# Kernel tuning notes

Measured on AMD Instinct MI355X. Metric: run time of the kernel, lower is better.

Reference implementation:

```python
import jax, jax.numpy as jnp
import numpy as np

DIM = 1024
NUM_EXPERTS = 8
N_TOKENS = 8192


def setup_inputs() -> dict:
    key = jax.random.key(0)
    ks = jax.random.split(key, 6)
    z_real = jax.random.normal(ks[0], (N_TOKENS, DIM), dtype=jnp.float32)
    z_imag = jax.random.normal(ks[1], (N_TOKENS, DIM), dtype=jnp.float32)
    # gate: nn.Linear(2*dim, E) -> weight [E, 2*dim], bias [E]
    Wg = jax.random.normal(ks[2], (NUM_EXPERTS, 2 * DIM), dtype=jnp.float32) * (1.0 / np.sqrt(2 * DIM))
    bg = jnp.zeros((NUM_EXPERTS,), dtype=jnp.float32)
    # experts: per-expert real/imag square weights [E, dim, dim] (nn.Linear layout: [out, in])
    Wr = jax.random.normal(ks[3], (NUM_EXPERTS, DIM, DIM), dtype=jnp.float32) * (1.0 / np.sqrt(DIM))
    Wi = jax.random.normal(ks[4], (NUM_EXPERTS, DIM, DIM), dtype=jnp.float32) * (1.0 / np.sqrt(DIM))
    return {"z_real": z_real, "z_imag": z_imag, "Wg": Wg, "bg": bg, "Wr": Wr, "Wi": Wi}


def reference(z_real, z_imag, Wg, bg, Wr, Wi):
    # gate over concat(real, imag)
    z_flat = jnp.concatenate([z_real, z_imag], axis=-1)            # [N, 2D]
    gates = jax.nn.softmax(z_flat @ Wg.T + bg, axis=-1)            # [N, E]
    # all-expert complex linear: y = x @ W^T with W [E, out, in]
    rr = jnp.einsum('ni,eoi->neo', z_real, Wr)                     # real @ Wr
    ii = jnp.einsum('ni,eoi->neo', z_imag, Wi)                     # imag @ Wi
    ri = jnp.einsum('ni,eoi->neo', z_imag, Wr)                     # imag @ Wr
    ir = jnp.einsum('ni,eoi->neo', z_real, Wi)                     # real @ Wi
    out_r = jnp.einsum('ne,neo->no', gates, rr - ii)               # [N, D]
    out_i = jnp.einsum('ne,neo->no', gates, ri + ir)               # [N, D]
    return jnp.stack([out_r, out_i], axis=0)                       # [2, N, D]
```

## Files before the change

### kernel.cpp

```cpp
#include <hip/hip_runtime.h>
#include <hip/hip_bf16.h>

#define NTOK 8192
#define DIM 1024
#define NEXP 8
#define NT 256
#define BK 64
#define NELEMZ ((size_t)NTOK * DIM)

typedef float f32x4 __attribute__((ext_vector_type(4)));
typedef short s16x8 __attribute__((ext_vector_type(8)));
typedef unsigned short u16;
typedef unsigned short u16x4 __attribute__((ext_vector_type(4)));

__device__ __forceinline__ u16 f2bf(float f) {
    __hip_bfloat16 h = __float2bfloat16(f);
    return *reinterpret_cast<u16*>(&h);
}

#define GLOAD16(gsrc, ldst)                                                     \
    __builtin_amdgcn_global_load_lds(                                           \
        (const __attribute__((address_space(1))) void*)(gsrc),                  \
        (__attribute__((address_space(3))) void*)(ldst), 16, 0, 0)

#define MFMA16(a, b, c) __builtin_amdgcn_mfma_f32_16x16x32_bf16((a), (b), (c), 0, 0, 0)

__global__ __launch_bounds__(256) void gates_kernel(
    const float* __restrict__ zr, const float* __restrict__ zi,
    const float* __restrict__ Wg, const float* __restrict__ bg,
    float* __restrict__ gT)
{
    const int wave = threadIdx.x >> 6, lane = threadIdx.x & 63;
    const int n = blockIdx.x * 4 + wave;

    float v[32];
    const float* zrp = zr + (size_t)n * DIM;
    const float* zip = zi + (size_t)n * DIM;
#pragma unroll
    for (int j = 0; j < 16; ++j) v[j] = zrp[j * 64 + lane];
#pragma unroll
    for (int j = 0; j < 16; ++j) v[16 + j] = zip[j * 64 + lane];

    float s[NEXP];
#pragma unroll
    for (int e = 0; e < NEXP; ++e) {
        const float* wrow = Wg + (size_t)e * (2 * DIM);
        float a = 0.f;
#pragma unroll
        for (int j = 0; j < 32; ++j) a += v[j] * wrow[j * 64 + lane];
#pragma unroll
        for (int m = 32; m; m >>= 1) a += __shfl_xor(a, m);
        s[e] = a + bg[e];
    }
    float mx = s[0];
#pragma unroll
    for (int e = 1; e < NEXP; ++e) mx = fmaxf(mx, s[e]);
    float p[NEXP], sum = 0.f;
#pragma unroll
    for (int e = 0; e < NEXP; ++e) { p[e] = expf(s[e] - mx); sum += p[e]; }
    const float inv = 1.f / sum;
    if (lane == 0) {
#pragma unroll
        for (int e = 0; e < NEXP; ++e) gT[(size_t)e * NTOK + n] = p[e] * inv;
    }
}

__global__ __launch_bounds__(256) void cvt4_kernel(
    const float* __restrict__ zr, const float* __restrict__ zi,
    const float* __restrict__ Wr, const float* __restrict__ Wi,
    u16* __restrict__ zr16, u16* __restrict__ zi16,
    u16* __restrict__ Wr16, u16* __restrict__ Wi16)
{
    const size_t total = NELEMZ / 4;
    for (size_t i = (size_t)blockIdx.x * 256 + threadIdx.x; i < total;
         i += (size_t)gridDim.x * 256) {
        f32x4 a = ((const f32x4*)zr)[i];
        f32x4 b = ((const f32x4*)zi)[i];
        f32x4 c = ((const f32x4*)Wr)[i];
        f32x4 d = ((const f32x4*)Wi)[i];
        u16x4 pa, pb, pc, pd;
#pragma unroll
        for (int j = 0; j < 4; ++j) {
            pa[j] = f2bf(a[j]); pb[j] = f2bf(b[j]);
            pc[j] = f2bf(c[j]); pd[j] = f2bf(d[j]);
        }
        ((u16x4*)zr16)[i] = pa;
        ((u16x4*)zi16)[i] = pb;
        ((u16x4*)Wr16)[i] = pc;
        ((u16x4*)Wi16)[i] = pd;
    }
}

__global__ __launch_bounds__(256, 2) void moe_gemm16(
    const u16* __restrict__ zr16, const u16* __restrict__ zi16,
    const u16* __restrict__ Wr16, const u16* __restrict__ Wi16,
    const float* __restrict__ gT, float* __restrict__ out)
{
    extern __shared__ u16 lds[];

    const int bid = blockIdx.x;
    const int xcd = bid & 7;
    const int loc = bid >> 3;
    const int bm = xcd * 8 + (loc >> 4);
    const int grp = loc & 15;
    const int bn = grp & 7;
    const int sel = grp >> 3;

    const int tid = threadIdx.x;
    const int lane = tid & 63;
    const int wid = tid >> 6;
    const int wr = wid >> 1;
    const int wc = wid & 1;

    int ar_g[4], br_g[4];
#pragma unroll
    for (int q = 0; q < 4; ++q) {
        const int idx = q * 256 + tid;
        const int row = idx >> 3;
        const int c = (idx & 7) ^ (row & 7);
        ar_g[q] = (bm * 128 + row) * DIM + c * 8;
        br_g[q] = (bn * 128 + row) * DIM + c * 8;
    }

    const int cg = lane >> 4;
    const int l7 = lane & 7;
    const int ach0 = (cg ^ l7) * 8;
    const int ach1 = ((4 + cg) ^ l7) * 8;
    const int abase = (wr * 64 + (lane & 15)) * BK;
    const int bbase = (wc * 64 + (lane & 15)) * BK;

    const int grow0 = bm * 128 + wr * 64 + ((lane >> 4) << 2);

    f32x4 acc[4][4], tot[4][4];
#pragma unroll
    for (int m = 0; m < 4; ++m)
#pragma unroll
        for (int n = 0; n < 4; ++n) {
            acc[m][n] = (f32x4){0.f, 0.f, 0.f, 0.f};
            tot[m][n] = (f32x4){0.f, 0.f, 0.f, 0.f};
        }

    const u16* Asrc = sel ? zi16 : zr16;
    const u16* Bseg = Wr16;
    f32x4 sgm[4];

#pragma unroll
    for (int q = 0; q < 4; ++q) GLOAD16(Asrc + ar_g[q], &lds[(q * 256 + tid) * 8]);
#pragma unroll
    for (int q = 0; q < 4; ++q) GLOAD16(Bseg + br_g[q], &lds[16384 + (q * 256 + tid) * 8]);
    asm volatile("s_waitcnt vmcnt(0)" ::: "memory");
    __builtin_amdgcn_s_barrier();

#pragma unroll 1
    for (int t = 0; t < NT; ++t) {
        if ((t & 15) == 0) {
            const int seg = t >> 4;
            if (t) {
#pragma unroll
                for (int m = 0; m < 4; ++m)
#pragma unroll
                    for (int n = 0; n < 4; ++n) {
#pragma unroll
                        for (int j = 0; j < 4; ++j)
                            tot[m][n][j] += sgm[m][j] * acc[m][n][j];
                        acc[m][n] = (f32x4){0.f, 0.f, 0.f, 0.f};
                    }
            }
            const int e = seg >> 1, half = seg & 1;
            const float sgn = (sel == 0 && half == 1) ? -1.f : 1.f;
#pragma unroll
            for (int m = 0; m < 4; ++m) {
                const f32x4 g = *(const f32x4*)&gT[(size_t)e * NTOK + grow0 + m * 16];
#pragma unroll
                for (int j = 0; j < 4; ++j) sgm[m][j] = sgn * g[j];
            }
        }
        const int t1 = t + 1;
        if ((t1 & 15) == 0) {
            const int seg = t1 >> 4;
            const int e = (seg >> 1) & 7;
            const int half = seg & 1;
            Asrc = (half ^ sel) ? zi16 : zr16;
            Bseg = (half ? Wi16 : Wr16) + (size_t)e * DIM * DIM;
        }
        const int kb = (t1 & 15) << 6;
        const int rs = t & 1;
        const int sa = (rs ^ 1) * 8192;
        const int sb = 16384 + (rs ^ 1) * 8192;
        const int ab = rs * 8192 + abase;
        const int bb = 16384 + rs * 8192 + bbase;

        GLOAD16(Asrc + ar_g[0] + kb, &lds[sa + (0 * 256 + tid) * 8]);
        GLOAD16(Asrc + ar_g[1] + kb, &lds[sa + (1 * 256 + tid) * 8]);
        GLOAD16(Asrc + ar_g[2] + kb, &lds[sa + (2 * 256 + tid) * 8]);
        GLOAD16(Asrc + ar_g[3] + kb, &lds[sa + (3 * 256 + tid) * 8]);
        GLOAD16(Bseg + br_g[0] + kb, &lds[sb + (0 * 256 + tid) * 8]);
        GLOAD16(Bseg + br_g[1] + kb, &lds[sb + (1 * 256 + tid) * 8]);
        GLOAD16(Bseg + br_g[2] + kb, &lds[sb + (2 * 256 + tid) * 8]);
        GLOAD16(Bseg + br_g[3] + kb, &lds[sb + (3 * 256 + tid) * 8]);

        s16x8 a0[4], b0[4];
#pragma unroll
        for (int m = 0; m < 4; ++m) a0[m] = *(const s16x8*)&lds[ab + m * 1024 + ach0];
#pragma unroll
        for (int n = 0; n < 4; ++n) b0[n] = *(const s16x8*)&lds[bb + n * 1024 + ach0];
        __builtin_amdgcn_s_setprio(1);
#pragma unroll
        for (int m = 0; m < 4; ++m)
#pragma unroll
            for (int n = 0; n < 4; ++n) acc[m][n] = MFMA16(a0[m], b0[n], acc[m][n]);
        __builtin_amdgcn_s_setprio(0);

        s16x8 a1[4], b1[4];
#pragma unroll
        for (int m = 0; m < 4; ++m) a1[m] = *(const s16x8*)&lds[ab + m * 1024 + ach1];
#pragma unroll
        for (int n = 0; n < 4; ++n) b1[n] = *(const s16x8*)&lds[bb + n * 1024 + ach1];
        __builtin_amdgcn_s_setprio(1);
#pragma unroll
        for (int m = 0; m < 4; ++m)
#pragma unroll
            for (int n = 0; n < 4; ++n) acc[m][n] = MFMA16(a1[m], b1[n], acc[m][n]);
        __builtin_amdgcn_s_setprio(0);

        asm volatile("s_waitcnt vmcnt(0) lgkmcnt(0)" ::: "memory");
        __builtin_amdgcn_s_barrier();
    }

#pragma unroll
    for (int m = 0; m < 4; ++m)
#pragma unroll
        for (int n = 0; n < 4; ++n)
#pragma unroll
            for (int j = 0; j < 4; ++j)
                tot[m][n][j] += sgm[m][j] * acc[m][n][j];

    float* op = out + (size_t)sel * NTOK * DIM;
    const int col0 = bn * 128 + wc * 64 + (lane & 15);
#pragma unroll
    for (int m = 0; m < 4; ++m)
#pragma unroll
        for (int n = 0; n < 4; ++n)
#pragma unroll
            for (int j = 0; j < 4; ++j)
                op[(size_t)(grow0 + m * 16 + j) * DIM + col0 + n * 16] = tot[m][n][j];
}

extern "C" void kernel_launch(void* const* d_in, const int* in_sizes, int n_in,
                              void* d_out, int out_size, void* d_ws, size_t ws_size,
                              hipStream_t stream) {
    const float* zr = (const float*)d_in[0];
    const float* zi = (const float*)d_in[1];
    const float* Wg = (const float*)d_in[2];
    const float* bg = (const float*)d_in[3];
    const float* Wr = (const float*)d_in[4];
    const float* Wi = (const float*)d_in[5];
    float* out = (float*)d_out;

    u16* zr16 = (u16*)d_ws;
    u16* zi16 = zr16 + NELEMZ;
    u16* Wr16 = zi16 + NELEMZ;
    u16* Wi16 = Wr16 + NELEMZ;
    float* gT = (float*)(Wi16 + NELEMZ);

    cvt4_kernel<<<2048, 256, 0, stream>>>(zr, zi, Wr, Wi, zr16, zi16, Wr16, Wi16);
    gates_kernel<<<NTOK / 4, 256, 0, stream>>>(zr, zi, Wg, bg, gT);

    hipFuncSetAttribute((const void*)moe_gemm16,
                        hipFuncAttributeMaxDynamicSharedMemorySize, 65536);
    moe_gemm16<<<1024, 256, 65536, stream>>>(zr16, zi16, Wr16, Wi16, gT, out);
}
```

Baseline: 580.4 us.

## Triple-buffer B tiles to prefetch weights two iterations ahead

Adds a third LDS buffer for the weight (B) tiles and issues their global-to-LDS loads two k-steps ahead, while A tiles stay double-buffered one step ahead. The per-iteration wait relaxes from vmcnt(0) to vmcnt(4), so the newest B loads can stay in flight across the barrier and more memory latency is hidden. The cost is dynamic LDS growing from 64KB to 80KB per block, which may limit how many blocks fit per CU, plus more complex buffer-index bookkeeping.

After: 582.2 us. Within noise of the previous version (+0.3%).

```diff
diff --git a/kernel.cpp b/kernel.cpp
--- a/kernel.cpp
+++ b/kernel.cpp
@@ -91,7 +91,7 @@
     }
 }
 
-__global__ __launch_bounds__(256, 2) void moe_gemm16(
+__global__ __launch_bounds__(256, 2) void moe_gemm17(
     const u16* __restrict__ zr16, const u16* __restrict__ zi16,
     const u16* __restrict__ Wr16, const u16* __restrict__ Wi16,
     const float* __restrict__ gT, float* __restrict__ out)
@@ -148,9 +148,12 @@
     for (int q = 0; q < 4; ++q) GLOAD16(Asrc + ar_g[q], &lds[(q * 256 + tid) * 8]);
 #pragma unroll
     for (int q = 0; q < 4; ++q) GLOAD16(Bseg + br_g[q], &lds[16384 + (q * 256 + tid) * 8]);
-    asm volatile("s_waitcnt vmcnt(0)" ::: "memory");
+#pragma unroll
+    for (int q = 0; q < 4; ++q) GLOAD16(Bseg + br_g[q] + BK, &lds[24576 + (q * 256 + tid) * 8]);
+    asm volatile("s_waitcnt vmcnt(4)" ::: "memory");
     __builtin_amdgcn_s_barrier();
 
+    int brs = 0;
 #pragma unroll 1
     for (int t = 0; t < NT; ++t) {
         if ((t & 15) == 0) {
@@ -175,29 +178,34 @@
                 for (int j = 0; j < 4; ++j) sgm[m][j] = sgn * g[j];
             }
         }
-        const int t1 = t + 1;
+        const int t1 = t + 1, t2 = t + 2;
         if ((t1 & 15) == 0) {
             const int seg = t1 >> 4;
-            const int e = (seg >> 1) & 7;
             const int half = seg & 1;
             Asrc = (half ^ sel) ? zi16 : zr16;
-            Bseg = (half ? Wi16 : Wr16) + (size_t)e * DIM * DIM;
-        }
-        const int kb = (t1 & 15) << 6;
+        }
+        if ((t2 & 15) == 0) {
+            const int seg = t2 >> 4;
+            const int e = (seg >> 1) & 7;
+            Bseg = ((seg & 1) ? Wi16 : Wr16) + (size_t)e * DIM * DIM;
+        }
+        const int ka1 = (t1 & 15) << 6;
+        const int kb2 = (t2 & 15) << 6;
         const int rs = t & 1;
+        const int bss = (brs == 0) ? 2 : brs - 1;
         const int sa = (rs ^ 1) * 8192;
-        const int sb = 16384 + (rs ^ 1) * 8192;
+        const int sb = 16384 + bss * 8192;
         const int ab = rs * 8192 + abase;
-        const int bb = 16384 + rs * 8192 + bbase;
-
-        GLOAD16(Asrc + ar_g[0] + kb, &lds[sa + (0 * 256 + tid) * 8]);
-        GLOAD16(Asrc + ar_g[1] + kb, &lds[sa + (1 * 256 + tid) * 8]);
-        GLOAD16(Asrc + ar_g[2] + kb, &lds[sa + (2 * 256 + tid) * 8]);
-        GLOAD16(Asrc + ar_g[3] + kb, &lds[sa + (3 * 256 + tid) * 8]);
-        GLOAD16(Bseg + br_g[0] + kb, &lds[sb + (0 * 256 + tid) * 8]);
-        GLOAD16(Bseg + br_g[1] + kb, &lds[sb + (1 * 256 + tid) * 8]);
-        GLOAD16(Bseg + br_g[2] + kb, &lds[sb + (2 * 256 + tid) * 8]);
-        GLOAD16(Bseg + br_g[3] + kb, &lds[sb + (3 * 256 + tid) * 8]);
+        const int bb = 16384 + brs * 8192 + bbase;
+
+        GLOAD16(Asrc + ar_g[0] + ka1, &lds[sa + (0 * 256 + tid) * 8]);
+        GLOAD16(Asrc + ar_g[1] + ka1, &lds[sa + (1 * 256 + tid) * 8]);
+        GLOAD16(Asrc + ar_g[2] + ka1, &lds[sa + (2 * 256 + tid) * 8]);
+        GLOAD16(Asrc + ar_g[3] + ka1, &lds[sa + (3 * 256 + tid) * 8]);
+        GLOAD16(Bseg + br_g[0] + kb2, &lds[sb + (0 * 256 + tid) * 8]);
+        GLOAD16(Bseg + br_g[1] + kb2, &lds[sb + (1 * 256 + tid) * 8]);
+        GLOAD16(Bseg + br_g[2] + kb2, &lds[sb + (2 * 256 + tid) * 8]);
+        GLOAD16(Bseg + br_g[3] + kb2, &lds[sb + (3 * 256 + tid) * 8]);
 
         s16x8 a0[4], b0[4];
 #pragma unroll
@@ -223,9 +231,12 @@
             for (int n = 0; n < 4; ++n) acc[m][n] = MFMA16(a1[m], b1[n], acc[m][n]);
         __builtin_amdgcn_s_setprio(0);
 
-        asm volatile("s_waitcnt vmcnt(0) lgkmcnt(0)" ::: "memory");
+        asm volatile("s_waitcnt vmcnt(4) lgkmcnt(0)" ::: "memory");
         __builtin_amdgcn_s_barrier();
-    }
+
+        brs = (brs == 2) ? 0 : brs + 1;
+    }
+    asm volatile("s_waitcnt vmcnt(0)" ::: "memory");
 
 #pragma unroll
     for (int m = 0; m < 4; ++m)
@@ -266,7 +277,7 @@
     cvt4_kernel<<<2048, 256, 0, stream>>>(zr, zi, Wr, Wi, zr16, zi16, Wr16, Wi16);
     gates_kernel<<<NTOK / 4, 256, 0, stream>>>(zr, zi, Wg, bg, gT);
 
-    hipFuncSetAttribute((const void*)moe_gemm16,
-                        hipFuncAttributeMaxDynamicSharedMemorySize, 65536);
-    moe_gemm16<<<1024, 256, 65536, stream>>>(zr16, zi16, Wr16, Wi16, gT, out);
-}
+    hipFuncSetAttribute((const void*)moe_gemm17,
+                        hipFuncAttributeMaxDynamicSharedMemorySize, 81920);
+    moe_gemm17<<<1024, 256, 81920, stream>>>(zr16, zi16, Wr16, Wi16, gT, out);
+}
```
